# Performance work log

Measured on AMD Instinct MI355X. Metric: run time of the kernel, lower is better.

## Reference

```python
import jax, jax.numpy as jnp
import numpy as np

N_IN, N_HIDDEN, N, K = 14, 256, 131072, 10

def _linear_params(key, n_in, n_out):
    kw, kb = jax.random.split(key)
    lim = 1.0 / np.sqrt(n_in)
    W = jax.random.uniform(kw, (n_in, n_out), jnp.float32, -lim, lim)
    b = jax.random.uniform(kb, (n_out,), jnp.float32, -lim, lim)
    return W, b

def setup_inputs() -> dict:
    key = jax.random.key(0)
    ks = jax.random.split(key, 8)
    towers = jax.random.normal(ks[0], (N, K, N_IN), jnp.float32)
    M1_w, M1_b = _linear_params(ks[1], N_IN + N_HIDDEN, N_HIDDEN)
    M2_w, M2_b = _linear_params(ks[2], N_HIDDEN, N_HIDDEN)
    M3_w, M3_b = _linear_params(ks[3], N_HIDDEN, N_HIDDEN)
    O1_w, O1_b = _linear_params(ks[4], N_IN + N_HIDDEN, N_HIDDEN)
    O2_w, O2_b = _linear_params(ks[5], N_HIDDEN, N_HIDDEN)
    O3_w, O3_b = _linear_params(ks[6], N_HIDDEN, 1)
    aggregate = jnp.zeros((1, N_HIDDEN), jnp.float32)
    return dict(towers=towers, aggregate=aggregate,
                M1_w=M1_w, M1_b=M1_b, M2_w=M2_w, M2_b=M2_b, M3_w=M3_w, M3_b=M3_b,
                O1_w=O1_w, O1_b=O1_b, O2_w=O2_w, O2_b=O2_b, O3_w=O3_w, O3_b=O3_b,
                k=K)

def reference(towers, aggregate,
              M1_w, M1_b, M2_w, M2_b, M3_w, M3_b,
              O1_w, O1_b, O2_w, O2_b, O3_w, O3_b, k):
    N_, K_, _ = towers.shape
    # flip along tower axis, then scan over K steps (top-down)
    tows = jnp.transpose(towers[:, ::-1, :], (1, 0, 2))  # (K, N, n_in)

    def mlp_M(x):
        h = jax.nn.relu(x @ M1_w + M1_b)
        h = jax.nn.relu(h @ M2_w + M2_b)
        return jax.nn.relu(h @ M3_w + M3_b)

    def mlp_O(x):
        h = jax.nn.relu(x @ O1_w + O1_b)
        h = jax.nn.relu(h @ O2_w + O2_b)
        return h @ O3_w + O3_b  # (N, 1)

    def step(carry, tow_k):
        summary, prod = carry
        x = jnp.concatenate([summary, tow_k], axis=1)  # (N, n_hidden + n_in)
        pred = jax.nn.sigmoid(mlp_O(x))[:, 0]
        new_summary = mlp_M(x)
        return (new_summary, prod * pred), None

    init_summary = jnp.broadcast_to(aggregate, (N_, aggregate.shape[1]))
    init_prod = jnp.ones((N_,), towers.dtype)
    (final_summary, prod), _ = jax.lax.scan(step, (init_summary, init_prod), tows)
    return prod  # (N,)
```

## Files before the change

kernel.cpp:

```cpp
#include <hip/hip_runtime.h>
#include <math.h>
#include <stdint.h>


typedef _Float16 half8 __attribute__((ext_vector_type(8)));
typedef __fp16 fp16x2 __attribute__((ext_vector_type(2)));
typedef float f32x4 __attribute__((ext_vector_type(4)));

constexpr int KS = 10;
constexpr int RSTR = 584;
constexpr float SPLIT_S = 2048.f;
constexpr float SPLIT_INV = 1.f / 2048.f;

__device__ __align__(16) _Float16 g_Wh[672 * 512];
__device__ __align__(16) _Float16 g_Wl[672 * 512];
__device__ __align__(16) uint4 g_park[2048u * 4u * 16u * 64u];

__global__ void prep_w(const float* __restrict__ O1w, const float* __restrict__ M1w,
                       const float* __restrict__ O2w, const float* __restrict__ M2w,
                       const float* __restrict__ M3w) {
  const int bid = blockIdx.x, l = threadIdx.x;
  const float* W; int Ksrc, f;
  if (bid < 144)      { W = O1w; Ksrc = 270; f = bid; }
  else if (bid < 288) { W = M1w; Ksrc = 270; f = bid - 144; }
  else if (bid < 416) { W = O2w; Ksrc = 256; f = bid - 288; }
  else if (bid < 544) { W = M2w; Ksrc = 256; f = bid - 416; }
  else                { W = M3w; Ksrc = 256; f = bid - 544; }
  const int c = f >> 4, nt = f & 15, g = l >> 4, s = l & 15;
  const int of = nt * 16 + s;
  union { half8 h; uint4 u; } hv, lv;
#pragma unroll
  for (int i = 0; i < 8; ++i) {
    const int k = c * 32 + g * 8 + i;
    const float w = (k < Ksrc) ? W[k * 256 + of] : 0.f;
    const _Float16 h = (_Float16)w;
    hv.h[i] = h;
    lv.h[i] = (_Float16)((w - (float)h) * SPLIT_S);
  }
  ((uint4*)g_Wh)[bid * 64 + l] = hv.u;
  ((uint4*)g_Wl)[bid * 64 + l] = lv.u;
}

__device__ __forceinline__ half8 as_half8(uint4 u) {
  union { uint4 u4; half8 h; } c; c.u4 = u; return c.h;
}
__device__ __forceinline__ f32x4 mfma16(half8 a, half8 b, f32x4 c) {
  return __builtin_amdgcn_mfma_f32_16x16x32_f16(a, b, c, 0, 0, 0);
}
__device__ __forceinline__ uint32_t h2bits(fp16x2 h) {
  union { fp16x2 h2; uint32_t u; } c; c.h2 = h; return c.u;
}

struct PK { uint2 hi, lo; };
__device__ __forceinline__ PK split4(float v0, float v1, float v2, float v3) {
  fp16x2 h01 = __builtin_amdgcn_cvt_pkrtz(v0, v1);
  fp16x2 h23 = __builtin_amdgcn_cvt_pkrtz(v2, v3);
  fp16x2 l01 = __builtin_amdgcn_cvt_pkrtz((v0 - (float)h01[0]) * SPLIT_S,
                                          (v1 - (float)h01[1]) * SPLIT_S);
  fp16x2 l23 = __builtin_amdgcn_cvt_pkrtz((v2 - (float)h23[0]) * SPLIT_S,
                                          (v3 - (float)h23[1]) * SPLIT_S);
  PK r;
  r.hi = make_uint2(h2bits(h01), h2bits(h23));
  r.lo = make_uint2(h2bits(l01), h2bits(l23));
  return r;
}
__device__ __forceinline__ void split1(float v, _Float16& h, _Float16& l) {
  h = (_Float16)v;
  l = (_Float16)((v - (float)h) * SPLIT_S);
}

__device__ __forceinline__ int xidx(int row, int i, int xr) {
  return row * RSTR + (i ^ xr);
}

__device__ __forceinline__ void zero44(f32x4 a1[4][4], f32x4 a2[4][4]) {
#pragma unroll
  for (int n = 0; n < 4; ++n)
#pragma unroll
    for (int sf = 0; sf < 4; ++sf) {
      a1[n][sf] = (f32x4){0.f, 0.f, 0.f, 0.f};
      a2[n][sf] = (f32x4){0.f, 0.f, 0.f, 0.f};
    }
}

template <int CHUNKS>
__device__ __forceinline__ void lgemm(f32x4 a1[4][4], f32x4 a2[4][4],
                                      const _Float16* __restrict__ Xs,
                                      const uint4* __restrict__ Wh,
                                      const uint4* __restrict__ Wl,
                                      int wu, int g, int s, int xr) {
#pragma unroll 1
  for (int c = 0; c < CHUNKS; ++c) {
    uint4 wh[4], wl[4];
#pragma unroll
    for (int n = 0; n < 4; ++n) {
      wh[n] = Wh[(c * 16 + 4 * wu + n) * 64];
      wl[n] = Wl[(c * 16 + 4 * wu + n) * 64];
    }
#pragma unroll
    for (int sf = 0; sf < 4; ++sf) {
      const _Float16* xp = Xs + xidx(16 * sf + s, c * 32 + g * 8, xr);
      half8 bh = *(const half8*)xp;
      half8 bl = *(const half8*)(xp + 288);
#pragma unroll
      for (int n = 0; n < 4; ++n) {
        a1[n][sf] = mfma16(as_half8(wh[n]), bh, a1[n][sf]);
        a2[n][sf] = mfma16(as_half8(wh[n]), bl, a2[n][sf]);
        a2[n][sf] = mfma16(as_half8(wl[n]), bh, a2[n][sf]);
      }
    }
  }
}

__device__ __forceinline__ void epi_write(const f32x4 a1[4][4], const f32x4 a2[4][4],
                                          const float* __restrict__ bias,
                                          _Float16* __restrict__ Xs,
                                          int wu, int g, int s, int xr) {
#pragma unroll
  for (int n = 0; n < 4; ++n) {
    const float4 bv = *(const float4*)(bias + (4 * wu + n) * 16 + 4 * g);
#pragma unroll
    for (int sf = 0; sf < 4; ++sf) {
      const float v0 = fmaxf(fmaf(a2[n][sf][0], SPLIT_INV, a1[n][sf][0]) + bv.x, 0.f);
      const float v1 = fmaxf(fmaf(a2[n][sf][1], SPLIT_INV, a1[n][sf][1]) + bv.y, 0.f);
      const float v2 = fmaxf(fmaf(a2[n][sf][2], SPLIT_INV, a1[n][sf][2]) + bv.z, 0.f);
      const float v3 = fmaxf(fmaf(a2[n][sf][3], SPLIT_INV, a1[n][sf][3]) + bv.w, 0.f);
      const PK p = split4(v0, v1, v2, v3);
      _Float16* yp = Xs + xidx(16 * sf + s, (4 * wu + n) * 16 + 4 * g, xr);
      *(uint2*)yp = p.hi;
      *(uint2*)(yp + 288) = p.lo;
    }
  }
}

__device__ __forceinline__ void epi_park(const f32x4 a1[4][4], const f32x4 a2[4][4],
                                         const float* __restrict__ bias,
                                         uint4* __restrict__ slot,
                                         int wu, int g, int l) {
#pragma unroll
  for (int n = 0; n < 4; ++n) {
    const float4 bv = *(const float4*)(bias + (4 * wu + n) * 16 + 4 * g);
#pragma unroll
    for (int p = 0; p < 2; ++p) {
      PK q[2];
#pragma unroll
      for (int h = 0; h < 2; ++h) {
        const int sf = 2 * p + h;
        const float v0 = fmaxf(fmaf(a2[n][sf][0], SPLIT_INV, a1[n][sf][0]) + bv.x, 0.f);
        const float v1 = fmaxf(fmaf(a2[n][sf][1], SPLIT_INV, a1[n][sf][1]) + bv.y, 0.f);
        const float v2 = fmaxf(fmaf(a2[n][sf][2], SPLIT_INV, a1[n][sf][2]) + bv.z, 0.f);
        const float v3 = fmaxf(fmaf(a2[n][sf][3], SPLIT_INV, a1[n][sf][3]) + bv.w, 0.f);
        q[h] = split4(v0, v1, v2, v3);
      }
      slot[(n * 2 + p) * 64 + l]     = make_uint4(q[0].hi.x, q[0].hi.y, q[1].hi.x, q[1].hi.y);
      slot[(8 + n * 2 + p) * 64 + l] = make_uint4(q[0].lo.x, q[0].lo.y, q[1].lo.x, q[1].lo.y);
    }
  }
}

__device__ __forceinline__ void unpark_write(const uint4 pk[16],
                                             _Float16* __restrict__ Xs,
                                             int wu, int g, int s, int xr) {
#pragma unroll
  for (int n = 0; n < 4; ++n)
#pragma unroll
    for (int p = 0; p < 2; ++p) {
      const uint4 hi = pk[n * 2 + p];
      const uint4 lo = pk[8 + n * 2 + p];
#pragma unroll
      for (int h = 0; h < 2; ++h) {
        const int sf = 2 * p + h;
        _Float16* yp = Xs + xidx(16 * sf + s, (4 * wu + n) * 16 + 4 * g, xr);
        *(uint2*)yp = h ? make_uint2(hi.z, hi.w) : make_uint2(hi.x, hi.y);
        *(uint2*)(yp + 288) = h ? make_uint2(lo.z, lo.w) : make_uint2(lo.x, lo.y);
      }
    }
}

__global__ __launch_bounds__(256, 2) void topdown_mfma(
    const float* __restrict__ towers, const float* __restrict__ aggregate,
    const float* __restrict__ O1b, const float* __restrict__ O2b,
    const float* __restrict__ O3w, const float* __restrict__ O3b,
    const float* __restrict__ M1b, const float* __restrict__ M2b,
    const float* __restrict__ M3b, float* __restrict__ out) {
  __shared__ __align__(16) _Float16 Xs[64 * RSTR];
  __shared__ __align__(16) float scr[64][4];
  const int t = threadIdx.x, l = t & 63;
  const int wu = __builtin_amdgcn_readfirstlane(t >> 6);
  const int g = l >> 4, s = l & 15;
  const int xr = s & 8;
  const int n0 = blockIdx.x * 64;
  uint4* park = g_park + ((size_t)blockIdx.x * 4 + (size_t)wu) * (16 * 64);

  for (int idx = t; idx < 64 * 288; idx += 256) {
    const int ss = idx / 288, f = idx - ss * 288;
    const float v = (f < 256) ? aggregate[f] : 0.f;
    _Float16 h, lo; split1(v, h, lo);
    const int p = xidx(ss, f, ss & 8);
    Xs[p] = h;
    Xs[p + 288] = lo;
  }

  float prod = 1.f;
  const float o3bias = O3b[0];
  f32x4 a1[4][4], a2[4][4];

  const uint4* WhL = (const uint4*)g_Wh + l;
  const uint4* WlL = (const uint4*)g_Wl + l;

  for (int kk = 0; kk < KS; ++kk) {
    const int tbase = (KS - 1 - kk) * 14;
    for (int idx = t; idx < 64 * 14; idx += 256) {
      const int ss = idx / 14, f = idx - ss * 14;
      const float v = towers[(size_t)(n0 + ss) * (KS * 14) + tbase + f];
      _Float16 h, lo; split1(v, h, lo);
      const int p = xidx(ss, 256 + f, ss & 8);
      Xs[p] = h;
      Xs[p + 288] = lo;
    }
    __syncthreads();

    zero44(a1, a2);
    lgemm<9>(a1, a2, Xs, WhL + 144 * 64, WlL + 144 * 64, wu, g, s, xr);
    epi_park(a1, a2, M1b, park, wu, g, l);

    zero44(a1, a2);
    lgemm<9>(a1, a2, Xs, WhL, WlL, wu, g, s, xr);
    __syncthreads();
    epi_write(a1, a2, O1b, Xs, wu, g, s, xr);
    __syncthreads();

    zero44(a1, a2);
    lgemm<8>(a1, a2, Xs, WhL + 288 * 64, WlL + 288 * 64, wu, g, s, xr);

    asm volatile("" ::: "memory");
    uint4 pk[16];
#pragma unroll
    for (int q = 0; q < 16; ++q) pk[q] = park[q * 64 + l];

    float tp[4] = {0.f, 0.f, 0.f, 0.f};
#pragma unroll
    for (int n = 0; n < 4; ++n) {
      const int ob = (4 * wu + n) * 16 + 4 * g;
      const float4 bv = *(const float4*)(O2b + ob);
      const float4 ov = *(const float4*)(O3w + ob);
      const float bb[4] = {bv.x, bv.y, bv.z, bv.w};
      const float oo[4] = {ov.x, ov.y, ov.z, ov.w};
#pragma unroll
      for (int sf = 0; sf < 4; ++sf)
#pragma unroll
        for (int r = 0; r < 4; ++r)
          tp[sf] += fmaxf(fmaf(a2[n][sf][r], SPLIT_INV, a1[n][sf][r]) + bb[r], 0.f) * oo[r];
    }
#pragma unroll
    for (int sf = 0; sf < 4; ++sf) {
      tp[sf] += __shfl_xor(tp[sf], 16);
      tp[sf] += __shfl_xor(tp[sf], 32);
    }
    if (g == 0) {
#pragma unroll
      for (int sf = 0; sf < 4; ++sf) scr[16 * sf + s][wu] = tp[sf];
    }
    __syncthreads();

    unpark_write(pk, Xs, wu, g, s, xr);
    if (t < 64) {
      const float4 sv = *(const float4*)(scr[t]);
      prod *= 1.f / (1.f + expf(-(sv.x + sv.y + sv.z + sv.w + o3bias)));
    }
    __syncthreads();

    zero44(a1, a2);
    lgemm<8>(a1, a2, Xs, WhL + 416 * 64, WlL + 416 * 64, wu, g, s, xr);
    __syncthreads();
    epi_write(a1, a2, M2b, Xs, wu, g, s, xr);
    __syncthreads();

    zero44(a1, a2);
    lgemm<8>(a1, a2, Xs, WhL + 544 * 64, WlL + 544 * 64, wu, g, s, xr);
    __syncthreads();
    epi_write(a1, a2, M3b, Xs, wu, g, s, xr);
  }

  if (t < 64) out[n0 + t] = prod;
}

extern "C" void kernel_launch(void* const* d_in, const int* in_sizes, int n_in,
                              void* d_out, int out_size, void* d_ws, size_t ws_size,
                              hipStream_t stream) {
  const float* towers    = (const float*)d_in[0];
  const float* aggregate = (const float*)d_in[1];
  const float* M1w = (const float*)d_in[2];
  const float* M1b = (const float*)d_in[3];
  const float* M2w = (const float*)d_in[4];
  const float* M2b = (const float*)d_in[5];
  const float* M3w = (const float*)d_in[6];
  const float* M3b = (const float*)d_in[7];
  const float* O1w = (const float*)d_in[8];
  const float* O1b = (const float*)d_in[9];
  const float* O2w = (const float*)d_in[10];
  const float* O2b = (const float*)d_in[11];
  const float* O3w = (const float*)d_in[12];
  const float* O3b = (const float*)d_in[13];
  float* out = (float*)d_out;

  prep_w<<<672, 64, 0, stream>>>(O1w, M1w, O2w, M2w, M3w);

  const int nblocks = out_size / 64;
  topdown_mfma<<<nblocks, 256, 0, stream>>>(towers, aggregate, O1b, O2b, O3w,
                                            O3b, M1b, M2b, M3b, out);
}
```

Baseline: 2.631 ms.

## Split output columns across eight waves per block and drop LDS XOR swizzle

Each block now runs 512 threads (8 waves). Every wave computes 2 of the 16 output tiles instead of 4, which halves its accumulator and weight registers and lets up to 4 blocks share a CU under the new launch bounds. The sigmoid reduction now sums eight per-wave partials, and the park buffer is resized to match. The XOR swizzle on LDS row indexing is also removed, which simplifies address math but may bring back LDS bank conflicts on the half8 reads. More waves per block also means each __syncthreads has more waves to wait for.

```diff
diff --git a/kernel.cpp b/kernel.cpp
--- a/kernel.cpp
+++ b/kernel.cpp
@@ -14,7 +14,7 @@
 
 __device__ __align__(16) _Float16 g_Wh[672 * 512];
 __device__ __align__(16) _Float16 g_Wl[672 * 512];
-__device__ __align__(16) uint4 g_park[2048u * 4u * 16u * 64u];
+__device__ __align__(16) uint4 g_park[2048u * 8u * 8u * 64u];
 
 __global__ void prep_w(const float* __restrict__ O1w, const float* __restrict__ M1w,
                        const float* __restrict__ O2w, const float* __restrict__ M2w,
@@ -69,13 +69,9 @@
   l = (_Float16)((v - (float)h) * SPLIT_S);
 }
 
-__device__ __forceinline__ int xidx(int row, int i, int xr) {
-  return row * RSTR + (i ^ xr);
-}
-
-__device__ __forceinline__ void zero44(f32x4 a1[4][4], f32x4 a2[4][4]) {
-#pragma unroll
-  for (int n = 0; n < 4; ++n)
+__device__ __forceinline__ void zero24(f32x4 a1[2][4], f32x4 a2[2][4]) {
+#pragma unroll
+  for (int n = 0; n < 2; ++n)
 #pragma unroll
     for (int sf = 0; sf < 4; ++sf) {
       a1[n][sf] = (f32x4){0.f, 0.f, 0.f, 0.f};
@@ -84,26 +80,26 @@
 }
 
 template <int CHUNKS>
-__device__ __forceinline__ void lgemm(f32x4 a1[4][4], f32x4 a2[4][4],
+__device__ __forceinline__ void lgemm(f32x4 a1[2][4], f32x4 a2[2][4],
                                       const _Float16* __restrict__ Xs,
                                       const uint4* __restrict__ Wh,
                                       const uint4* __restrict__ Wl,
-                                      int wu, int g, int s, int xr) {
+                                      int wu, int g, int s) {
 #pragma unroll 1
   for (int c = 0; c < CHUNKS; ++c) {
-    uint4 wh[4], wl[4];
-#pragma unroll
-    for (int n = 0; n < 4; ++n) {
-      wh[n] = Wh[(c * 16 + 4 * wu + n) * 64];
-      wl[n] = Wl[(c * 16 + 4 * wu + n) * 64];
+    uint4 wh[2], wl[2];
+#pragma unroll
+    for (int n = 0; n < 2; ++n) {
+      wh[n] = Wh[(c * 16 + 2 * wu + n) * 64];
+      wl[n] = Wl[(c * 16 + 2 * wu + n) * 64];
     }
 #pragma unroll
     for (int sf = 0; sf < 4; ++sf) {
-      const _Float16* xp = Xs + xidx(16 * sf + s, c * 32 + g * 8, xr);
+      const _Float16* xp = Xs + (16 * sf + s) * RSTR + c * 32 + g * 8;
       half8 bh = *(const half8*)xp;
       half8 bl = *(const half8*)(xp + 288);
 #pragma unroll
-      for (int n = 0; n < 4; ++n) {
+      for (int n = 0; n < 2; ++n) {
         a1[n][sf] = mfma16(as_half8(wh[n]), bh, a1[n][sf]);
         a2[n][sf] = mfma16(as_half8(wh[n]), bl, a2[n][sf]);
         a2[n][sf] = mfma16(as_half8(wl[n]), bh, a2[n][sf]);
@@ -112,13 +108,13 @@
   }
 }
 
-__device__ __forceinline__ void epi_write(const f32x4 a1[4][4], const f32x4 a2[4][4],
+__device__ __forceinline__ void epi_write(const f32x4 a1[2][4], const f32x4 a2[2][4],
                                           const float* __restrict__ bias,
                                           _Float16* __restrict__ Xs,
-                                          int wu, int g, int s, int xr) {
-#pragma unroll
-  for (int n = 0; n < 4; ++n) {
-    const float4 bv = *(const float4*)(bias + (4 * wu + n) * 16 + 4 * g);
+                                          int wu, int g, int s) {
+#pragma unroll
+  for (int n = 0; n < 2; ++n) {
+    const float4 bv = *(const float4*)(bias + (2 * wu + n) * 16 + 4 * g);
 #pragma unroll
     for (int sf = 0; sf < 4; ++sf) {
       const float v0 = fmaxf(fmaf(a2[n][sf][0], SPLIT_INV, a1[n][sf][0]) + bv.x, 0.f);
@@ -126,20 +122,20 @@
       const float v2 = fmaxf(fmaf(a2[n][sf][2], SPLIT_INV, a1[n][sf][2]) + bv.z, 0.f);
       const float v3 = fmaxf(fmaf(a2[n][sf][3], SPLIT_INV, a1[n][sf][3]) + bv.w, 0.f);
       const PK p = split4(v0, v1, v2, v3);
-      _Float16* yp = Xs + xidx(16 * sf + s, (4 * wu + n) * 16 + 4 * g, xr);
+      _Float16* yp = Xs + (16 * sf + s) * RSTR + (2 * wu + n) * 16 + 4 * g;
       *(uint2*)yp = p.hi;
       *(uint2*)(yp + 288) = p.lo;
     }
   }
 }
 
-__device__ __forceinline__ void epi_park(const f32x4 a1[4][4], const f32x4 a2[4][4],
+__device__ __forceinline__ void epi_park(const f32x4 a1[2][4], const f32x4 a2[2][4],
                                          const float* __restrict__ bias,
                                          uint4* __restrict__ slot,
                                          int wu, int g, int l) {
 #pragma unroll
-  for (int n = 0; n < 4; ++n) {
-    const float4 bv = *(const float4*)(bias + (4 * wu + n) * 16 + 4 * g);
+  for (int n = 0; n < 2; ++n) {
+    const float4 bv = *(const float4*)(bias + (2 * wu + n) * 16 + 4 * g);
 #pragma unroll
     for (int p = 0; p < 2; ++p) {
       PK q[2];
@@ -153,95 +149,92 @@
         q[h] = split4(v0, v1, v2, v3);
       }
       slot[(n * 2 + p) * 64 + l]     = make_uint4(q[0].hi.x, q[0].hi.y, q[1].hi.x, q[1].hi.y);
-      slot[(8 + n * 2 + p) * 64 + l] = make_uint4(q[0].lo.x, q[0].lo.y, q[1].lo.x, q[1].lo.y);
-    }
-  }
-}
-
-__device__ __forceinline__ void unpark_write(const uint4 pk[16],
+      slot[(4 + n * 2 + p) * 64 + l] = make_uint4(q[0].lo.x, q[0].lo.y, q[1].lo.x, q[1].lo.y);
+    }
+  }
+}
+
+__device__ __forceinline__ void unpark_write(const uint4 pk[8],
                                              _Float16* __restrict__ Xs,
-                                             int wu, int g, int s, int xr) {
-#pragma unroll
-  for (int n = 0; n < 4; ++n)
+                                             int wu, int g, int s) {
+#pragma unroll
+  for (int n = 0; n < 2; ++n)
 #pragma unroll
     for (int p = 0; p < 2; ++p) {
       const uint4 hi = pk[n * 2 + p];
-      const uint4 lo = pk[8 + n * 2 + p];
+      const uint4 lo = pk[4 + n * 2 + p];
 #pragma unroll
       for (int h = 0; h < 2; ++h) {
         const int sf = 2 * p + h;
-        _Float16* yp = Xs + xidx(16 * sf + s, (4 * wu + n) * 16 + 4 * g, xr);
+        _Float16* yp = Xs + (16 * sf + s) * RSTR + (2 * wu + n) * 16 + 4 * g;
         *(uint2*)yp = h ? make_uint2(hi.z, hi.w) : make_uint2(hi.x, hi.y);
         *(uint2*)(yp + 288) = h ? make_uint2(lo.z, lo.w) : make_uint2(lo.x, lo.y);
       }
     }
 }
 
-__global__ __launch_bounds__(256, 2) void topdown_mfma(
+__global__ __launch_bounds__(512, 4) void topdown_mfma(
     const float* __restrict__ towers, const float* __restrict__ aggregate,
     const float* __restrict__ O1b, const float* __restrict__ O2b,
     const float* __restrict__ O3w, const float* __restrict__ O3b,
     const float* __restrict__ M1b, const float* __restrict__ M2b,
     const float* __restrict__ M3b, float* __restrict__ out) {
   __shared__ __align__(16) _Float16 Xs[64 * RSTR];
-  __shared__ __align__(16) float scr[64][4];
+  __shared__ __align__(16) float scr[64][8];
   const int t = threadIdx.x, l = t & 63;
   const int wu = __builtin_amdgcn_readfirstlane(t >> 6);
   const int g = l >> 4, s = l & 15;
-  const int xr = s & 8;
   const int n0 = blockIdx.x * 64;
-  uint4* park = g_park + ((size_t)blockIdx.x * 4 + (size_t)wu) * (16 * 64);
-
-  for (int idx = t; idx < 64 * 288; idx += 256) {
+  uint4* park = g_park + ((size_t)blockIdx.x * 8 + (size_t)wu) * (8 * 64);
+
+  for (int idx = t; idx < 64 * 288; idx += 512) {
     const int ss = idx / 288, f = idx - ss * 288;
     const float v = (f < 256) ? aggregate[f] : 0.f;
     _Float16 h, lo; split1(v, h, lo);
-    const int p = xidx(ss, f, ss & 8);
-    Xs[p] = h;
-    Xs[p + 288] = lo;
+    Xs[ss * RSTR + f] = h;
+    Xs[ss * RSTR + 288 + f] = lo;
   }
 
   float prod = 1.f;
   const float o3bias = O3b[0];
-  f32x4 a1[4][4], a2[4][4];
+  f32x4 a1[2][4], a2[2][4];
 
   const uint4* WhL = (const uint4*)g_Wh + l;
   const uint4* WlL = (const uint4*)g_Wl + l;
 
   for (int kk = 0; kk < KS; ++kk) {
     const int tbase = (KS - 1 - kk) * 14;
-    for (int idx = t; idx < 64 * 14; idx += 256) {
+    for (int idx = t; idx < 64 * 14; idx += 512) {
       const int ss = idx / 14, f = idx - ss * 14;
       const float v = towers[(size_t)(n0 + ss) * (KS * 14) + tbase + f];
       _Float16 h, lo; split1(v, h, lo);
-      const int p = xidx(ss, 256 + f, ss & 8);
-      Xs[p] = h;
-      Xs[p + 288] = lo;
-    }
-    __syncthreads();
-
-    zero44(a1, a2);
-    lgemm<9>(a1, a2, Xs, WhL + 144 * 64, WlL + 144 * 64, wu, g, s, xr);
+      Xs[ss * RSTR + 256 + f] = h;
+      Xs[ss * RSTR + 288 + 256 + f] = lo;
+    }
+    __syncthreads();
+
+    zero24(a1, a2);
+    lgemm<9>(a1, a2, Xs, WhL + 144 * 64, WlL + 144 * 64, wu, g, s);
     epi_park(a1, a2, M1b, park, wu, g, l);
 
-    zero44(a1, a2);
-    lgemm<9>(a1, a2, Xs, WhL, WlL, wu, g, s, xr);
-    __syncthreads();
-    epi_write(a1, a2, O1b, Xs, wu, g, s, xr);
-    __syncthreads();
-
-    zero44(a1, a2);
-    lgemm<8>(a1, a2, Xs, WhL + 288 * 64, WlL + 288 * 64, wu, g, s, xr);
+    zero24(a1, a2);
+    lgemm<9>(a1, a2, Xs, WhL, WlL, wu, g, s);
+    __syncthreads();
+    epi_write(a1, a2, O1b, Xs, wu, g, s);
+    __syncthreads();
+
+    zero24(a1, a2);
+    lgemm<8>(a1, a2, Xs, WhL + 288 * 64, WlL + 288 * 64, wu, g, s);
 
     asm volatile("" ::: "memory");
-    uint4 pk[16];
-#pragma unroll
-    for (int q = 0; q < 16; ++q) pk[q] = park[q * 64 + l];
+    uint4 pk[8];
+#pragma unroll
+    for (int q = 0; q < 8; ++q) pk[q] = park[q * 64 + l];
 
     float tp[4] = {0.f, 0.f, 0.f, 0.f};
 #pragma unroll
-    for (int n = 0; n < 4; ++n) {
-      const int ob = (4 * wu + n) * 16 + 4 * g;
+    for (int n = 0; n < 2; ++n) {
+      const int ob = (2 * wu + n) * 16 + 4 * g;
       const float4 bv = *(const float4*)(O2b + ob);
       const float4 ov = *(const float4*)(O3w + ob);
       const float bb[4] = {bv.x, bv.y, bv.z, bv.w};
@@ -263,23 +256,26 @@
     }
     __syncthreads();
 
-    unpark_write(pk, Xs, wu, g, s, xr);
+    unpark_write(pk, Xs, wu, g, s);
     if (t < 64) {
-      const float4 sv = *(const float4*)(scr[t]);
-      prod *= 1.f / (1.f + expf(-(sv.x + sv.y + sv.z + sv.w + o3bias)));
-    }
-    __syncthreads();
-
-    zero44(a1, a2);
-    lgemm<8>(a1, a2, Xs, WhL + 416 * 64, WlL + 416 * 64, wu, g, s, xr);
-    __syncthreads();
-    epi_write(a1, a2, M2b, Xs, wu, g, s, xr);
-    __syncthreads();
-
-    zero44(a1, a2);
-    lgemm<8>(a1, a2, Xs, WhL + 544 * 64, WlL + 544 * 64, wu, g, s, xr);
-    __syncthreads();
-    epi_write(a1, a2, M3b, Xs, wu, g, s, xr);
+      const float4 s0 = *(const float4*)(scr[t]);
+      const float4 s1 = *(const float4*)(scr[t] + 4);
+      const float tt = ((s0.x + s0.y) + (s0.z + s0.w)) +
+                       ((s1.x + s1.y) + (s1.z + s1.w)) + o3bias;
+      prod *= 1.f / (1.f + expf(-tt));
+    }
+    __syncthreads();
+
+    zero24(a1, a2);
+    lgemm<8>(a1, a2, Xs, WhL + 416 * 64, WlL + 416 * 64, wu, g, s);
+    __syncthreads();
+    epi_write(a1, a2, M2b, Xs, wu, g, s);
+    __syncthreads();
+
+    zero24(a1, a2);
+    lgemm<8>(a1, a2, Xs, WhL + 544 * 64, WlL + 544 * 64, wu, g, s);
+    __syncthreads();
+    epi_write(a1, a2, M3b, Xs, wu, g, s);
   }
 
   if (t < 64) out[n0 + t] = prod;
@@ -307,6 +303,6 @@
   prep_w<<<672, 64, 0, stream>>>(O1w, M1w, O2w, M2w, M3w);
 
   const int nblocks = out_size / 64;
-  topdown_mfma<<<nblocks, 256, 0, stream>>>(towers, aggregate, O1b, O2b, O3w,
+  topdown_mfma<<<nblocks, 512, 0, stream>>>(towers, aggregate, O1b, O2b, O3w,
                                             O3b, M1b, M2b, M3b, out);
 }
```

Result: faster. 2.408 ms (-8.5%).
